# Optimization experiments

Hardware: AMD Instinct MI355X
Metric: run time of the kernel (lower is better)

## Reference

```python
import jax, jax.numpy as jnp
import numpy as np
import itertools

LUT_DIM = 33  # 33x33x33 color LUT, as in Generator3DLUT_zero(dim=33)


def setup_inputs() -> dict:
    key = jax.random.key(0)
    k1, k2 = jax.random.split(key)
    # RGB image batch in [0,1]: [B, 3, H, W]
    x = jax.random.uniform(k1, (4, 3, 1080, 1920), dtype=jnp.float32)
    # Learned LUT parameter: [3, dim, dim, dim] (channels, b-axis, g-axis, r-axis)
    LUT = jax.random.normal(k2, (3, LUT_DIM, LUT_DIM, LUT_DIM), dtype=jnp.float32)
    return {"x": x, "LUT": LUT}


def _trilinear_lut(x, LUT, dim):
    # x: [B,3,H,W] in [0,1]; LUT: [3,dim,dim,dim] indexed [channel, b, g, r]
    # (r varies fastest, matching the original CUDA trilinear_forward kernel
    #  where flat index = r + g*dim + b*dim*dim).
    scaled = jnp.clip(x, 0.0, 1.0) * (dim - 1)          # [B,3,H,W]
    idx = jnp.clip(jnp.floor(scaled).astype(jnp.int32), 0, dim - 2)
    frac = scaled - idx.astype(scaled.dtype)            # in [0,1]
    r_id, g_id, b_id = idx[:, 0], idx[:, 1], idx[:, 2]   # each [B,H,W]
    fr, fg, fb = frac[:, 0], frac[:, 1], frac[:, 2]      # each [B,H,W]

    out = jnp.zeros_like(x)  # [B,3,H,W]
    for dr, dg, db in itertools.product((0, 1), repeat=3):  # 8 corners
        w = (jnp.where(dr, fr, 1.0 - fr)
             * jnp.where(dg, fg, 1.0 - fg)
             * jnp.where(db, fb, 1.0 - fb))               # [B,H,W]
        corner = LUT[:, b_id + db, g_id + dg, r_id + dr]  # [3,B,H,W] gather
        out = out + w[:, None] * jnp.transpose(corner, (1, 0, 2, 3))
    return out


def reference(x, LUT):
    return _trilinear_lut(x, LUT, LUT_DIM)
```

## Files before the change

### kernel.cpp

```cpp
#include <hip/hip_runtime.h>

#define DIM  33
#define DIM2 1089
#define DIM3 35937
#define HW   2073600
#define HW4  518400
#define NPIX 8294400
#define GROUPS (NPIX / 4)
#define LDS_BYTES (DIM3 * 4)
#define MAIN_BLOCKS  256
#define MAIN_THREADS 1024
#define NB_MAX ((3 * DIM3 + 255) / 256)

typedef float vf4 __attribute__((ext_vector_type(4)));

#define TBL_OFF 64

__device__ __forceinline__ float ub(unsigned v, int b) {
    return (float)((v >> (8 * b)) & 0xffu);
}

__global__ __launch_bounds__(256) void lut_maxabs_blocks(
        const float* __restrict__ lut, float* __restrict__ slots) {
    __shared__ float red[4];
    int i = blockIdx.x * 256 + threadIdx.x;
    float m = 0.0f;
    if (i < 3 * DIM3) m = fabsf(lut[i]);
#pragma unroll
    for (int off = 32; off > 0; off >>= 1)
        m = fmaxf(m, __shfl_down(m, off, 64));
    if ((threadIdx.x & 63) == 0) red[threadIdx.x >> 6] = m;
    __syncthreads();
    if (threadIdx.x == 0)
        slots[blockIdx.x] = fmaxf(fmaxf(red[0], red[1]), fmaxf(red[2], red[3]));
}

extern __shared__ unsigned s_tbl[];

__global__ __launch_bounds__(MAIN_THREADS, 1) void lut_apply_lds(
        const float* __restrict__ x, const float* __restrict__ lut,
        const float* __restrict__ slots, float* __restrict__ out) {
    __shared__ float red[16];

    float m = 0.0f;
    if (threadIdx.x < NB_MAX) m = slots[threadIdx.x];
#pragma unroll
    for (int off = 32; off > 0; off >>= 1)
        m = fmaxf(m, __shfl_down(m, off, 64));
    if ((threadIdx.x & 63) == 0) red[threadIdx.x >> 6] = m;
    __syncthreads();
    float mx = red[0];
#pragma unroll
    for (int j = 1; j < 16; ++j) mx = fmaxf(mx, red[j]);
    mx = fmaxf(mx, 1e-20f);

    const float inv = 127.0f / mx;
    for (int i = threadIdx.x; i < DIM3; i += MAIN_THREADS) {
        int q0 = min(max(__float2int_rn(lut[i]            * inv) + 128, 0), 255);
        int q1 = min(max(__float2int_rn(lut[i + DIM3]     * inv) + 128, 0), 255);
        int q2 = min(max(__float2int_rn(lut[i + 2 * DIM3] * inv) + 128, 0), 255);
        s_tbl[i] = (unsigned)q0 | ((unsigned)q1 << 8) | ((unsigned)q2 << 16);
    }
    __syncthreads();

    const float s_   = mx * (1.0f / 127.0f);
    const float bias = -128.0f * s_;

    for (int g = blockIdx.x * MAIN_THREADS + threadIdx.x; g < GROUPS;
         g += MAIN_BLOCKS * MAIN_THREADS) {
        int n   = g / HW4;
        int rem = g - n * HW4;
        size_t base = (size_t)n * (size_t)(3 * HW) + (size_t)rem * 4;

        const vf4 rv = __builtin_nontemporal_load((const vf4*)(x + base));
        const vf4 gv = __builtin_nontemporal_load((const vf4*)(x + base + HW));
        const vf4 bv = __builtin_nontemporal_load((const vf4*)(x + base + 2 * (size_t)HW));

        float oa[4], ob[4], oc[4];
#pragma unroll
        for (int k = 0; k < 4; ++k) {
            float rs = fminf(fmaxf(rv[k], 0.0f), 1.0f) * 32.0f;
            float gs = fminf(fmaxf(gv[k], 0.0f), 1.0f) * 32.0f;
            float bs = fminf(fmaxf(bv[k], 0.0f), 1.0f) * 32.0f;
            int ri = min((int)rs, 31);
            int gi = min((int)gs, 31);
            int bi = min((int)bs, 31);
            float fr = rs - (float)ri;
            float fg = gs - (float)gi;
            float fb = bs - (float)bi;

            int i00 = bi * DIM2 + gi * DIM + ri;
            unsigned c000 = s_tbl[i00];
            unsigned c001 = s_tbl[i00 + 1];
            unsigned c010 = s_tbl[i00 + DIM];
            unsigned c011 = s_tbl[i00 + DIM + 1];
            unsigned c100 = s_tbl[i00 + DIM2];
            unsigned c101 = s_tbl[i00 + DIM2 + 1];
            unsigned c110 = s_tbl[i00 + DIM2 + DIM];
            unsigned c111 = s_tbl[i00 + DIM2 + DIM + 1];

            float wr1 = fr, wr0 = 1.0f - fr;
            float wg1 = fg, wg0 = 1.0f - fg;
            float wb1 = fb, wb0 = 1.0f - fb;
            float wb0g0 = wb0 * wg0, wb0g1 = wb0 * wg1;
            float wb1g0 = wb1 * wg0, wb1g1 = wb1 * wg1;
            float w000 = wb0g0 * wr0, w001 = wb0g0 * wr1;
            float w010 = wb0g1 * wr0, w011 = wb0g1 * wr1;
            float w100 = wb1g0 * wr0, w101 = wb1g0 * wr1;
            float w110 = wb1g1 * wr0, w111 = wb1g1 * wr1;

            float a0, a1, a2;
            a0 =      w000 * ub(c000, 0);
            a1 =      w000 * ub(c000, 1);
            a2 =      w000 * ub(c000, 2);
            a0 = fmaf(w001,  ub(c001, 0), a0);
            a1 = fmaf(w001,  ub(c001, 1), a1);
            a2 = fmaf(w001,  ub(c001, 2), a2);
            a0 = fmaf(w010,  ub(c010, 0), a0);
            a1 = fmaf(w010,  ub(c010, 1), a1);
            a2 = fmaf(w010,  ub(c010, 2), a2);
            a0 = fmaf(w011,  ub(c011, 0), a0);
            a1 = fmaf(w011,  ub(c011, 1), a1);
            a2 = fmaf(w011,  ub(c011, 2), a2);
            a0 = fmaf(w100,  ub(c100, 0), a0);
            a1 = fmaf(w100,  ub(c100, 1), a1);
            a2 = fmaf(w100,  ub(c100, 2), a2);
            a0 = fmaf(w101,  ub(c101, 0), a0);
            a1 = fmaf(w101,  ub(c101, 1), a1);
            a2 = fmaf(w101,  ub(c101, 2), a2);
            a0 = fmaf(w110,  ub(c110, 0), a0);
            a1 = fmaf(w110,  ub(c110, 1), a1);
            a2 = fmaf(w110,  ub(c110, 2), a2);
            a0 = fmaf(w111,  ub(c111, 0), a0);
            a1 = fmaf(w111,  ub(c111, 1), a1);
            a2 = fmaf(w111,  ub(c111, 2), a2);

            oa[k] = fmaf(s_, a0, bias);
            ob[k] = fmaf(s_, a1, bias);
            oc[k] = fmaf(s_, a2, bias);
        }
        vf4 s0 = {oa[0], oa[1], oa[2], oa[3]};
        vf4 s1 = {ob[0], ob[1], ob[2], ob[3]};
        vf4 s2 = {oc[0], oc[1], oc[2], oc[3]};
        __builtin_nontemporal_store(s0, (vf4*)(out + base));
        __builtin_nontemporal_store(s1, (vf4*)(out + base + HW));
        __builtin_nontemporal_store(s2, (vf4*)(out + base + 2 * (size_t)HW));
    }
}

union F4H { vf4 f4; _Float16 h[8]; };

__global__ __launch_bounds__(256) void pack_lut8_kernel(
        const float* __restrict__ lut, vf4* __restrict__ lut8) {
    int i = blockIdx.x * blockDim.x + threadIdx.x;
    if (i >= DIM3) return;
    int b   = i / DIM2;
    int rem = i - b * DIM2;
    int g   = rem / DIM;
    int r   = rem - g * DIM;
    int b1 = min(b + 1, DIM - 1);
    int g1 = min(g + 1, DIM - 1);
    int r1 = min(r + 1, DIM - 1);
    _Float16 h[32];
#pragma unroll
    for (int db = 0; db < 2; ++db)
#pragma unroll
        for (int dg = 0; dg < 2; ++dg)
#pragma unroll
            for (int dr = 0; dr < 2; ++dr) {
                int bb = db ? b1 : b;
                int gg = dg ? g1 : g;
                int rr = dr ? r1 : r;
                int base = bb * DIM2 + gg * DIM + rr;
                int ci = ((db * 2 + dg) * 2 + dr) * 3;
                h[ci + 0] = (_Float16)lut[base];
                h[ci + 1] = (_Float16)lut[base + DIM3];
                h[ci + 2] = (_Float16)lut[base + 2 * DIM3];
            }
#pragma unroll
    for (int k = 24; k < 32; ++k) h[k] = (_Float16)0.0f;
    const vf4* hv = (const vf4*)h;
    vf4* dst = lut8 + (size_t)i * 4;
    dst[0] = hv[0]; dst[1] = hv[1]; dst[2] = hv[2]; dst[3] = hv[3];
}

__global__ __launch_bounds__(256) void lut_apply_fp16x8(
        const float* __restrict__ x, const vf4* __restrict__ lut8,
        float* __restrict__ out) {
    int i4 = blockIdx.x * blockDim.x + threadIdx.x;
    if (i4 >= NPIX / 4) return;
    int n   = i4 / HW4;
    int rem = i4 - n * HW4;
    size_t base = (size_t)n * (size_t)(3 * HW) + (size_t)rem * 4;
    const vf4 rv = __builtin_nontemporal_load((const vf4*)(x + base));
    const vf4 gv = __builtin_nontemporal_load((const vf4*)(x + base + HW));
    const vf4 bv = __builtin_nontemporal_load((const vf4*)(x + base + 2 * (size_t)HW));
    float oa[4], ob[4], oc[4];
#pragma unroll
    for (int k = 0; k < 4; ++k) {
        float rs = fminf(fmaxf(rv[k], 0.0f), 1.0f) * 32.0f;
        float gs = fminf(fmaxf(gv[k], 0.0f), 1.0f) * 32.0f;
        float bs = fminf(fmaxf(bv[k], 0.0f), 1.0f) * 32.0f;
        int ri = min((int)rs, 31);
        int gi = min((int)gs, 31);
        int bi = min((int)bs, 31);
        float fr = rs - (float)ri;
        float fg = gs - (float)gi;
        float fb = bs - (float)bi;
        const vf4* e = lut8 + (size_t)(bi * DIM2 + gi * DIM + ri) * 4;
        F4H q0, q1, q2;
        q0.f4 = e[0]; q1.f4 = e[1]; q2.f4 = e[2];
        float c[24];
#pragma unroll
        for (int j = 0; j < 8; ++j) {
            c[j] = (float)q0.h[j]; c[8 + j] = (float)q1.h[j]; c[16 + j] = (float)q2.h[j];
        }
        float wr[2] = {1.0f - fr, fr};
        float wg[2] = {1.0f - fg, fg};
        float wb[2] = {1.0f - fb, fb};
        float a0 = 0.0f, a1 = 0.0f, a2 = 0.0f;
#pragma unroll
        for (int db = 0; db < 2; ++db)
#pragma unroll
            for (int dg = 0; dg < 2; ++dg) {
                float wbg = wb[db] * wg[dg];
#pragma unroll
                for (int dr = 0; dr < 2; ++dr) {
                    float w = wbg * wr[dr];
                    int ci = ((db * 2 + dg) * 2 + dr) * 3;
                    a0 = fmaf(w, c[ci + 0], a0);
                    a1 = fmaf(w, c[ci + 1], a1);
                    a2 = fmaf(w, c[ci + 2], a2);
                }
            }
        oa[k] = a0; ob[k] = a1; oc[k] = a2;
    }
    vf4 s0 = {oa[0], oa[1], oa[2], oa[3]};
    vf4 s1 = {ob[0], ob[1], ob[2], ob[3]};
    vf4 s2 = {oc[0], oc[1], oc[2], oc[3]};
    __builtin_nontemporal_store(s0, (vf4*)(out + base));
    __builtin_nontemporal_store(s1, (vf4*)(out + base + HW));
    __builtin_nontemporal_store(s2, (vf4*)(out + base + 2 * (size_t)HW));
}

extern "C" void kernel_launch(void* const* d_in, const int* in_sizes, int n_in,
                              void* d_out, int out_size, void* d_ws, size_t ws_size,
                              hipStream_t stream) {
    const float* x   = (const float*)d_in[0];
    const float* lut = (const float*)d_in[1];
    float* out = (float*)d_out;

    float* slots = (float*)((char*)d_ws + TBL_OFF);

    static hipError_t attr_err = hipFuncSetAttribute(
        (const void*)lut_apply_lds,
        hipFuncAttributeMaxDynamicSharedMemorySize, LDS_BYTES);
    hipError_t err2 = hipFuncSetAttribute(
        (const void*)lut_apply_lds,
        hipFuncAttributeMaxDynamicSharedMemorySize, LDS_BYTES);

    if (attr_err == hipSuccess && err2 == hipSuccess) {
        lut_maxabs_blocks<<<NB_MAX, 256, 0, stream>>>(lut, slots);
        lut_apply_lds<<<MAIN_BLOCKS, MAIN_THREADS, LDS_BYTES, stream>>>(
            x, lut, slots, out);
    } else {
        vf4* lut8 = (vf4*)((char*)d_ws + TBL_OFF);
        pack_lut8_kernel<<<(DIM3 + 255) / 256, 256, 0, stream>>>(lut, lut8);
        lut_apply_fp16x8<<<(GROUPS + 255) / 256, 256, 0, stream>>>(x, lut8, out);
    }
}
```

Baseline: 188.1 us.

## Split LUT apply per output channel with small byte tables in LDS

Each block now handles a single output channel and quantizes only that channel's LUT plane into a 36 KB byte table in static shared memory, instead of one 144 KB packed table per 1024-thread block. This allows several smaller blocks per CU and cuts per-pixel arithmetic to one interpolation. In exchange, every block reloads all three input channels, so input reads are tripled unless the cache absorbs them. The fp16 fallback path and the dynamic-LDS attribute setup are removed.

```diff
diff --git a/kernel.cpp b/kernel.cpp
--- a/kernel.cpp
+++ b/kernel.cpp
@@ -7,17 +7,22 @@
 #define HW4  518400
 #define NPIX 8294400
 #define GROUPS (NPIX / 4)
-#define LDS_BYTES (DIM3 * 4)
-#define MAIN_BLOCKS  256
-#define MAIN_THREADS 1024
 #define NB_MAX ((3 * DIM3 + 255) / 256)
+
+#define APPLY_THREADS 512
+#define BLOCKS_PER_CH 340
+#define APPLY_BLOCKS  (3 * BLOCKS_PER_CH)
+#define CH_STRIDE     (BLOCKS_PER_CH * APPLY_THREADS)
+#define NW ((DIM3 + 3) / 4)
 
 typedef float vf4 __attribute__((ext_vector_type(4)));
 
 #define TBL_OFF 64
 
-__device__ __forceinline__ float ub(unsigned v, int b) {
-    return (float)((v >> (8 * b)) & 0xffu);
+__device__ __forceinline__ size_t pix_base(int g) {
+    int n   = g / HW4;
+    int rem = g - n * HW4;
+    return (size_t)n * (size_t)(3 * HW) + (size_t)rem * 4;
 }
 
 __global__ __launch_bounds__(256) void lut_maxabs_blocks(
@@ -35,12 +40,14 @@
         slots[blockIdx.x] = fmaxf(fmaxf(red[0], red[1]), fmaxf(red[2], red[3]));
 }
 
-extern __shared__ unsigned s_tbl[];
-
-__global__ __launch_bounds__(MAIN_THREADS, 1) void lut_apply_lds(
+__global__ __launch_bounds__(APPLY_THREADS) void lut_apply_ch(
         const float* __restrict__ x, const float* __restrict__ lut,
         const float* __restrict__ slots, float* __restrict__ out) {
-    __shared__ float red[16];
+    __shared__ unsigned tbl32[NW];
+    __shared__ float red[APPLY_THREADS / 64];
+
+    const int ch = (int)(blockIdx.x % 3u);
+    const int cb = (int)(blockIdx.x / 3u);
 
     float m = 0.0f;
     if (threadIdx.x < NB_MAX) m = slots[threadIdx.x];
@@ -51,32 +58,38 @@
     __syncthreads();
     float mx = red[0];
 #pragma unroll
-    for (int j = 1; j < 16; ++j) mx = fmaxf(mx, red[j]);
+    for (int j = 1; j < APPLY_THREADS / 64; ++j) mx = fmaxf(mx, red[j]);
     mx = fmaxf(mx, 1e-20f);
 
     const float inv = 127.0f / mx;
-    for (int i = threadIdx.x; i < DIM3; i += MAIN_THREADS) {
-        int q0 = min(max(__float2int_rn(lut[i]            * inv) + 128, 0), 255);
-        int q1 = min(max(__float2int_rn(lut[i + DIM3]     * inv) + 128, 0), 255);
-        int q2 = min(max(__float2int_rn(lut[i + 2 * DIM3] * inv) + 128, 0), 255);
-        s_tbl[i] = (unsigned)q0 | ((unsigned)q1 << 8) | ((unsigned)q2 << 16);
+    const float* __restrict__ lch = lut + (size_t)ch * DIM3;
+    for (int w = threadIdx.x; w < NW; w += APPLY_THREADS) {
+        int c0 = w * 4;
+        unsigned v = 0;
+#pragma unroll
+        for (int j = 0; j < 4; ++j) {
+            int c = c0 + j;
+            int q = 0;
+            if (c < DIM3)
+                q = min(max(__float2int_rn(lch[c] * inv) + 128, 0), 255);
+            v |= (unsigned)q << (8 * j);
+        }
+        tbl32[w] = v;
     }
     __syncthreads();
 
+    const unsigned char* __restrict__ tbl = (const unsigned char*)tbl32;
     const float s_   = mx * (1.0f / 127.0f);
     const float bias = -128.0f * s_;
+    const size_t chOff = (size_t)ch * HW;
 
-    for (int g = blockIdx.x * MAIN_THREADS + threadIdx.x; g < GROUPS;
-         g += MAIN_BLOCKS * MAIN_THREADS) {
-        int n   = g / HW4;
-        int rem = g - n * HW4;
-        size_t base = (size_t)n * (size_t)(3 * HW) + (size_t)rem * 4;
-
+    for (int g = cb * APPLY_THREADS + (int)threadIdx.x; g < GROUPS; g += CH_STRIDE) {
+        size_t base = pix_base(g);
         const vf4 rv = __builtin_nontemporal_load((const vf4*)(x + base));
         const vf4 gv = __builtin_nontemporal_load((const vf4*)(x + base + HW));
         const vf4 bv = __builtin_nontemporal_load((const vf4*)(x + base + 2 * (size_t)HW));
 
-        float oa[4], ob[4], oc[4];
+        float oo[4];
 #pragma unroll
         for (int k = 0; k < 4; ++k) {
             float rs = fminf(fmaxf(rv[k], 0.0f), 1.0f) * 32.0f;
@@ -90,14 +103,14 @@
             float fb = bs - (float)bi;
 
             int i00 = bi * DIM2 + gi * DIM + ri;
-            unsigned c000 = s_tbl[i00];
-            unsigned c001 = s_tbl[i00 + 1];
-            unsigned c010 = s_tbl[i00 + DIM];
-            unsigned c011 = s_tbl[i00 + DIM + 1];
-            unsigned c100 = s_tbl[i00 + DIM2];
-            unsigned c101 = s_tbl[i00 + DIM2 + 1];
-            unsigned c110 = s_tbl[i00 + DIM2 + DIM];
-            unsigned c111 = s_tbl[i00 + DIM2 + DIM + 1];
+            float c000 = (float)tbl[i00];
+            float c001 = (float)tbl[i00 + 1];
+            float c010 = (float)tbl[i00 + DIM];
+            float c011 = (float)tbl[i00 + DIM + 1];
+            float c100 = (float)tbl[i00 + DIM2];
+            float c101 = (float)tbl[i00 + DIM2 + 1];
+            float c110 = (float)tbl[i00 + DIM2 + DIM];
+            float c111 = (float)tbl[i00 + DIM2 + DIM + 1];
 
             float wr1 = fr, wr0 = 1.0f - fr;
             float wg1 = fg, wg0 = 1.0f - fg;
@@ -109,138 +122,21 @@
             float w100 = wb1g0 * wr0, w101 = wb1g0 * wr1;
             float w110 = wb1g1 * wr0, w111 = wb1g1 * wr1;
 
-            float a0, a1, a2;
-            a0 =      w000 * ub(c000, 0);
-            a1 =      w000 * ub(c000, 1);
-            a2 =      w000 * ub(c000, 2);
-            a0 = fmaf(w001,  ub(c001, 0), a0);
-            a1 = fmaf(w001,  ub(c001, 1), a1);
-            a2 = fmaf(w001,  ub(c001, 2), a2);
-            a0 = fmaf(w010,  ub(c010, 0), a0);
-            a1 = fmaf(w010,  ub(c010, 1), a1);
-            a2 = fmaf(w010,  ub(c010, 2), a2);
-            a0 = fmaf(w011,  ub(c011, 0), a0);
-            a1 = fmaf(w011,  ub(c011, 1), a1);
-            a2 = fmaf(w011,  ub(c011, 2), a2);
-            a0 = fmaf(w100,  ub(c100, 0), a0);
-            a1 = fmaf(w100,  ub(c100, 1), a1);
-            a2 = fmaf(w100,  ub(c100, 2), a2);
-            a0 = fmaf(w101,  ub(c101, 0), a0);
-            a1 = fmaf(w101,  ub(c101, 1), a1);
-            a2 = fmaf(w101,  ub(c101, 2), a2);
-            a0 = fmaf(w110,  ub(c110, 0), a0);
-            a1 = fmaf(w110,  ub(c110, 1), a1);
-            a2 = fmaf(w110,  ub(c110, 2), a2);
-            a0 = fmaf(w111,  ub(c111, 0), a0);
-            a1 = fmaf(w111,  ub(c111, 1), a1);
-            a2 = fmaf(w111,  ub(c111, 2), a2);
+            float a;
+            a =      w000 * c000;
+            a = fmaf(w001,  c001, a);
+            a = fmaf(w010,  c010, a);
+            a = fmaf(w011,  c011, a);
+            a = fmaf(w100,  c100, a);
+            a = fmaf(w101,  c101, a);
+            a = fmaf(w110,  c110, a);
+            a = fmaf(w111,  c111, a);
 
-            oa[k] = fmaf(s_, a0, bias);
-            ob[k] = fmaf(s_, a1, bias);
-            oc[k] = fmaf(s_, a2, bias);
+            oo[k] = fmaf(s_, a, bias);
         }
-        vf4 s0 = {oa[0], oa[1], oa[2], oa[3]};
-        vf4 s1 = {ob[0], ob[1], ob[2], ob[3]};
-        vf4 s2 = {oc[0], oc[1], oc[2], oc[3]};
-        __builtin_nontemporal_store(s0, (vf4*)(out + base));
-        __builtin_nontemporal_store(s1, (vf4*)(out + base + HW));
-        __builtin_nontemporal_store(s2, (vf4*)(out + base + 2 * (size_t)HW));
+        vf4 s0 = {oo[0], oo[1], oo[2], oo[3]};
+        __builtin_nontemporal_store(s0, (vf4*)(out + base + chOff));
     }
-}
-
-union F4H { vf4 f4; _Float16 h[8]; };
-
-__global__ __launch_bounds__(256) void pack_lut8_kernel(
-        const float* __restrict__ lut, vf4* __restrict__ lut8) {
-    int i = blockIdx.x * blockDim.x + threadIdx.x;
-    if (i >= DIM3) return;
-    int b   = i / DIM2;
-    int rem = i - b * DIM2;
-    int g   = rem / DIM;
-    int r   = rem - g * DIM;
-    int b1 = min(b + 1, DIM - 1);
-    int g1 = min(g + 1, DIM - 1);
-    int r1 = min(r + 1, DIM - 1);
-    _Float16 h[32];
-#pragma unroll
-    for (int db = 0; db < 2; ++db)
-#pragma unroll
-        for (int dg = 0; dg < 2; ++dg)
-#pragma unroll
-            for (int dr = 0; dr < 2; ++dr) {
-                int bb = db ? b1 : b;
-                int gg = dg ? g1 : g;
-                int rr = dr ? r1 : r;
-                int base = bb * DIM2 + gg * DIM + rr;
-                int ci = ((db * 2 + dg) * 2 + dr) * 3;
-                h[ci + 0] = (_Float16)lut[base];
-                h[ci + 1] = (_Float16)lut[base + DIM3];
-                h[ci + 2] = (_Float16)lut[base + 2 * DIM3];
-            }
-#pragma unroll
-    for (int k = 24; k < 32; ++k) h[k] = (_Float16)0.0f;
-    const vf4* hv = (const vf4*)h;
-    vf4* dst = lut8 + (size_t)i * 4;
-    dst[0] = hv[0]; dst[1] = hv[1]; dst[2] = hv[2]; dst[3] = hv[3];
-}
-
-__global__ __launch_bounds__(256) void lut_apply_fp16x8(
-        const float* __restrict__ x, const vf4* __restrict__ lut8,
-        float* __restrict__ out) {
-    int i4 = blockIdx.x * blockDim.x + threadIdx.x;
-    if (i4 >= NPIX / 4) return;
-    int n   = i4 / HW4;
-    int rem = i4 - n * HW4;
-    size_t base = (size_t)n * (size_t)(3 * HW) + (size_t)rem * 4;
-    const vf4 rv = __builtin_nontemporal_load((const vf4*)(x + base));
-    const vf4 gv = __builtin_nontemporal_load((const vf4*)(x + base + HW));
-    const vf4 bv = __builtin_nontemporal_load((const vf4*)(x + base + 2 * (size_t)HW));
-    float oa[4], ob[4], oc[4];
-#pragma unroll
-    for (int k = 0; k < 4; ++k) {
-        float rs = fminf(fmaxf(rv[k], 0.0f), 1.0f) * 32.0f;
-        float gs = fminf(fmaxf(gv[k], 0.0f), 1.0f) * 32.0f;
-        float bs = fminf(fmaxf(bv[k], 0.0f), 1.0f) * 32.0f;
-        int ri = min((int)rs, 31);
-        int gi = min((int)gs, 31);
-        int bi = min((int)bs, 31);
-        float fr = rs - (float)ri;
-        float fg = gs - (float)gi;
-        float fb = bs - (float)bi;
-        const vf4* e = lut8 + (size_t)(bi * DIM2 + gi * DIM + ri) * 4;
-        F4H q0, q1, q2;
-        q0.f4 = e[0]; q1.f4 = e[1]; q2.f4 = e[2];
-        float c[24];
-#pragma unroll
-        for (int j = 0; j < 8; ++j) {
-            c[j] = (float)q0.h[j]; c[8 + j] = (float)q1.h[j]; c[16 + j] = (float)q2.h[j];
-        }
-        float wr[2] = {1.0f - fr, fr};
-        float wg[2] = {1.0f - fg, fg};
-        float wb[2] = {1.0f - fb, fb};
-        float a0 = 0.0f, a1 = 0.0f, a2 = 0.0f;
-#pragma unroll
-        for (int db = 0; db < 2; ++db)
-#pragma unroll
-            for (int dg = 0; dg < 2; ++dg) {
-                float wbg = wb[db] * wg[dg];
-#pragma unroll
-                for (int dr = 0; dr < 2; ++dr) {
-                    float w = wbg * wr[dr];
-                    int ci = ((db * 2 + dg) * 2 + dr) * 3;
-                    a0 = fmaf(w, c[ci + 0], a0);
-                    a1 = fmaf(w, c[ci + 1], a1);
-                    a2 = fmaf(w, c[ci + 2], a2);
-                }
-            }
-        oa[k] = a0; ob[k] = a1; oc[k] = a2;
-    }
-    vf4 s0 = {oa[0], oa[1], oa[2], oa[3]};
-    vf4 s1 = {ob[0], ob[1], ob[2], ob[3]};
-    vf4 s2 = {oc[0], oc[1], oc[2], oc[3]};
-    __builtin_nontemporal_store(s0, (vf4*)(out + base));
-    __builtin_nontemporal_store(s1, (vf4*)(out + base + HW));
-    __builtin_nontemporal_store(s2, (vf4*)(out + base + 2 * (size_t)HW));
 }
 
 extern "C" void kernel_launch(void* const* d_in, const int* in_sizes, int n_in,
@@ -252,20 +148,6 @@
 
     float* slots = (float*)((char*)d_ws + TBL_OFF);
 
-    static hipError_t attr_err = hipFuncSetAttribute(
-        (const void*)lut_apply_lds,
-        hipFuncAttributeMaxDynamicSharedMemorySize, LDS_BYTES);
-    hipError_t err2 = hipFuncSetAttribute(
-        (const void*)lut_apply_lds,
-        hipFuncAttributeMaxDynamicSharedMemorySize, LDS_BYTES);
-
-    if (attr_err == hipSuccess && err2 == hipSuccess) {
-        lut_maxabs_blocks<<<NB_MAX, 256, 0, stream>>>(lut, slots);
-        lut_apply_lds<<<MAIN_BLOCKS, MAIN_THREADS, LDS_BYTES, stream>>>(
-            x, lut, slots, out);
-    } else {
-        vf4* lut8 = (vf4*)((char*)d_ws + TBL_OFF);
-        pack_lut8_kernel<<<(DIM3 + 255) / 256, 256, 0, stream>>>(lut, lut8);
-        lut_apply_fp16x8<<<(GROUPS + 255) / 256, 256, 0, stream>>>(x, lut8, out);
-    }
+    lut_maxabs_blocks<<<NB_MAX, 256, 0, stream>>>(lut, slots);
+    lut_apply_ch<<<APPLY_BLOCKS, APPLY_THREADS, 0, stream>>>(x, lut, slots, out);
 }
```

Result: slower. 339.3 us (+80.4%).
